# Performance work log

Hardware: AMD Instinct MI355X
Metric: run time of the kernel (lower is better)

Reference implementation:

```python
import jax, jax.numpy as jnp
import numpy as np

E = 1024
H = 16
D = E // H  # head dim


def setup_inputs() -> dict:
    key = jax.random.key(0)
    ks = jax.random.split(key, 8)
    N, L = 4, 2048
    x = jax.random.normal(ks[0], (N, L, E), dtype=jnp.float32)
    attn_mask = jnp.zeros((N, L), dtype=jnp.float32)  # additive mask
    s = 0.02
    Wq = jax.random.normal(ks[1], (E, E), dtype=jnp.float32) * s
    bq = jnp.zeros((E,), dtype=jnp.float32)
    Wk = jax.random.normal(ks[2], (E, E), dtype=jnp.float32) * s
    bk = jnp.zeros((E,), dtype=jnp.float32)
    Wv = jax.random.normal(ks[3], (E, E), dtype=jnp.float32) * s
    bv = jnp.zeros((E,), dtype=jnp.float32)
    return {"x": x, "attn_mask": attn_mask, "Wq": Wq, "bq": bq,
            "Wk": Wk, "bk": bk, "Wv": Wv, "bv": bv}


def _to_heads(t):
    N, L, _ = t.shape
    return t.reshape(N, L, H, D).transpose(0, 2, 1, 3)  # [N,H,L,D]


def reference(x, attn_mask, Wq, bq, Wk, bk, Wv, bv):
    # Linear projections (torch Linear: x @ W.T + b)
    Q = _to_heads(x @ Wq.T + bq) * (1.0 / jnp.sqrt(jnp.float32(D)))
    K = _to_heads(x @ Wk.T + bk)
    V = _to_heads(x @ Wv.T + bv)
    scores = jnp.einsum('nhqd,nhkd->nhqk', Q, K) + attn_mask[:, None, None, :]
    attn = jax.nn.softmax(scores, axis=-1)  # dropout p=0 -> identity
    out = jnp.einsum('nhqk,nhkd->nhqd', attn, V)  # [N,H,L,D]
    N, _, L, _ = out.shape
    return out.transpose(0, 2, 1, 3).reshape(N, L, E)
```

## Files before the change

kernel.cpp:

```cpp
#include <hip/hip_runtime.h>

#define DEV __device__ __forceinline__

typedef unsigned short u16;
typedef __attribute__((ext_vector_type(8))) __bf16 bf16x8;
typedef __attribute__((ext_vector_type(4))) float f32x4;
typedef __attribute__((ext_vector_type(16))) float f32x16;

#define LOG2E 1.44269504088896340736f

DEV u16 f2bf(float f) {
  union { float f; unsigned u; } v; v.f = f;
  unsigned r = v.u + 0x7FFFu + ((v.u >> 16) & 1u);
  return (u16)(r >> 16);
}

DEV float exp2_fast(float x) {
#if __has_builtin(__builtin_amdgcn_exp2f)
  return __builtin_amdgcn_exp2f(x);
#else
  return exp2f(x);
#endif
}

DEV float xor32_f(float v) { return __shfl_xor(v, 32, 64); }
DEV unsigned xor32_u(unsigned v) {
  return (unsigned)__shfl_xor((int)v, 32, 64);
}
DEV unsigned cvtpk_b(float lo, float hi) {
  union { float f; unsigned u; } a, b;
  a.f = lo; b.f = hi;
  return __builtin_amdgcn_perm(b.u + 0x8000u, a.u + 0x8000u, 0x07060302u);
}
DEV float bperm_f(int srclane, float v) {
  union { float f; int i; } u;
  u.f = v;
  u.i = __builtin_amdgcn_ds_bpermute(srclane * 4, u.i);
  return u.f;
}

template <typename T>
DEV void gload_lds16(const T* g, T* l) {
  __builtin_amdgcn_global_load_lds(
      (const __attribute__((address_space(1))) void*)(g),
      (__attribute__((address_space(3))) void*)(l),
      16, 0, 0);
}

DEV bf16x8 ldfrag(const u16* p) { return *(const bf16x8*)p; }

DEV void cast8(const float* __restrict__ in, u16* __restrict__ out) {
  float4 a = ((const float4*)in)[0];
  float4 b = ((const float4*)in)[1];
  uint4 o;
  o.x = (unsigned)f2bf(a.x) | ((unsigned)f2bf(a.y) << 16);
  o.y = (unsigned)f2bf(a.z) | ((unsigned)f2bf(a.w) << 16);
  o.z = (unsigned)f2bf(b.x) | ((unsigned)f2bf(b.y) << 16);
  o.w = (unsigned)f2bf(b.z) | ((unsigned)f2bf(b.w) << 16);
  *(uint4*)out = o;
}

__global__ __launch_bounds__(256) void prep_kernel(
    const float* __restrict__ x, const float* __restrict__ Wq,
    const float* __restrict__ Wk, const float* __restrict__ Wv,
    const float* __restrict__ mask,
    u16* __restrict__ xb, u16* __restrict__ wb, float* __restrict__ mlog) {
  const int i = blockIdx.x * 256 + threadIdx.x;
  const int NX = 8192 * 1024 / 8;
  const int NW = 1024 * 1024 / 8;
  if (i < NX) {
    cast8(x + (long)i * 8, xb + (long)i * 8);
  } else if (i < NX + 3 * NW) {
    int j = i - NX;
    int sel = j / NW;
    int jj = j - sel * NW;
    const float* W = (sel == 0) ? Wq : (sel == 1) ? Wk : Wv;
    cast8(W + (long)jj * 8, wb + (long)j * 8);
  } else {
    int j = i - NX - 3 * NW;
    float4 a = ((const float4*)mask)[2 * j];
    float4 b = ((const float4*)mask)[2 * j + 1];
    a.x *= LOG2E; a.y *= LOG2E; a.z *= LOG2E; a.w *= LOG2E;
    b.x *= LOG2E; b.y *= LOG2E; b.z *= LOG2E; b.w *= LOG2E;
    ((float4*)mlog)[2 * j] = a;
    ((float4*)mlog)[2 * j + 1] = b;
  }
}

__global__ __launch_bounds__(256) void qkv_gemm(
    const u16* __restrict__ xb, const u16* __restrict__ wb,
    const float* __restrict__ bq, const float* __restrict__ bk, const float* __restrict__ bv,
    u16* __restrict__ qb, u16* __restrict__ kb, u16* __restrict__ vtb) {
  __shared__ u16 As[128 * 64];
  __shared__ u16 Bs[128 * 64];
  const int t = threadIdx.x, lane = t & 63, w = t >> 6;
  const int wm = w >> 1, wn = w & 1;
  const int m0 = blockIdx.x * 128;
  const int cb = blockIdx.y;
  const int wsel = cb >> 3;
  const int n0 = (cb & 7) * 128;
  const u16* W = wb + wsel * (1024 * 1024);
  const float* bias = (wsel == 0) ? bq : (wsel == 1) ? bk : bv;
  const float scale = (wsel == 0) ? 0.125f * LOG2E : 1.0f;

  f32x4 acc[4][4];
  const f32x4 z4 = {0.f, 0.f, 0.f, 0.f};
  for (int i = 0; i < 4; ++i)
    for (int j = 0; j < 4; ++j) acc[i][j] = z4;

  const int srow = w * 32 + (lane >> 3);
  const int scol = (lane & 7) * 8;

  for (int k0 = 0; k0 < 1024; k0 += 64) {
    __syncthreads();
    for (int i = 0; i < 4; ++i) {
      gload_lds16(xb + (m0 + srow + i * 8) * 1024 + k0 + scol, &As[w * 2048 + i * 512]);
      gload_lds16(W + (n0 + srow + i * 8) * 1024 + k0 + scol, &Bs[w * 2048 + i * 512]);
    }
    __syncthreads();
    for (int ks = 0; ks < 2; ++ks) {
      bf16x8 a[4], b[4];
      for (int mi = 0; mi < 4; ++mi)
        a[mi] = ldfrag(&As[(wm * 64 + mi * 16 + (lane & 15)) * 64 + ks * 32 + (lane >> 4) * 8]);
      for (int ni = 0; ni < 4; ++ni)
        b[ni] = ldfrag(&Bs[(wn * 64 + ni * 16 + (lane & 15)) * 64 + ks * 32 + (lane >> 4) * 8]);
      for (int mi = 0; mi < 4; ++mi)
        for (int ni = 0; ni < 4; ++ni)
          acc[mi][ni] = __builtin_amdgcn_mfma_f32_16x16x32_bf16(a[mi], b[ni], acc[mi][ni], 0, 0, 0);
    }
  }
  if (wsel == 2) {
    for (int ni = 0; ni < 4; ++ni) {
      int col = n0 + wn * 64 + ni * 16 + (lane & 15);
      float bv_ = bias[col];
      int h = col >> 6, d = col & 63;
      for (int mi = 0; mi < 4; ++mi) {
        int gm = m0 + wm * 64 + mi * 16 + (lane >> 4) * 4;
        int nn = gm >> 11, lq = gm & 2047;
        ushort4 pk;
        pk.x = f2bf(acc[mi][ni][0] + bv_);
        pk.y = f2bf(acc[mi][ni][1] + bv_);
        pk.z = f2bf(acc[mi][ni][2] + bv_);
        pk.w = f2bf(acc[mi][ni][3] + bv_);
        *(ushort4*)(vtb + ((long)((nn << 4) + h) * 64 + d) * 2048 + lq) = pk;
      }
    }
  } else {
    u16* dst = (wsel == 0) ? qb : kb;
    for (int ni = 0; ni < 4; ++ni) {
      int col = n0 + wn * 64 + ni * 16 + (lane & 15);
      float bv_ = bias[col];
      int h = col >> 6, d = col & 63;
      for (int mi = 0; mi < 4; ++mi) {
        for (int r = 0; r < 4; ++r) {
          int gm = m0 + wm * 64 + mi * 16 + (lane >> 4) * 4 + r;
          int nn = gm >> 11, lq = gm & 2047;
          float val = acc[mi][ni][r] * scale + bv_;
          dst[(((nn << 4) + h) * 2048 + lq) * 64 + d] = f2bf(val);
        }
      }
    }
  }
}

__global__ __launch_bounds__(256) void flash_attn(
    const u16* __restrict__ qb, const u16* __restrict__ kb, const u16* __restrict__ vtb,
    const float* __restrict__ mlog, float* __restrict__ out) {
  __shared__ u16 SM[4][64 * 64];
  __shared__ float MK[2048];

  const int t = threadIdx.x, lane = t & 63, w = t >> 6;
  const int hi = lane >> 5, l31 = lane & 31;
  const int bid = blockIdx.x;
  const int swz = (bid & 7) * 128 + (bid >> 3);
  const int q0 = (swz & 15) * 128;
  const int head = swz >> 4;
  const int n = head >> 4, h = head & 15;

  const u16* qh = qb + head * (2048 * 64);
  const u16* kh = kb + head * (2048 * 64);
  const u16* vth = vtb + head * (64 * 2048);
  const float* mrow = mlog + n * 2048;

  const int srow8 = lane >> 3;
  const int scolsw = ((lane & 7) ^ srow8) * 8;
  const int rsw = (lane & 7) * 8;
  int fcolB[4];
  for (int dk = 0; dk < 4; ++dk) fcolB[dk] = (16 * dk + 8 * hi) ^ rsw;

  u16* QL = &SM[0][0];
  for (int i = 0; i < 4; ++i)
    gload_lds16(qh + (q0 + w * 32 + i * 8 + srow8) * 64 + scolsw, &QL[(w * 32 + i * 8) * 64]);
  for (int i = 0; i < 2; ++i) {
    int chunk = w * 2 + i;
    gload_lds16(mrow + chunk * 256 + lane * 4, &MK[chunk * 256]);
  }
  __syncthreads();
  bf16x8 qf[4];
  for (int dk = 0; dk < 4; ++dk)
    qf[dk] = ldfrag(&QL[(w * 32 + l31) * 64 + fcolB[dk]]);
  __syncthreads();

  {
    gload_lds16(kh + (w * 16 + srow8) * 64 + scolsw, &SM[0][w * 1024]);
    gload_lds16(kh + (w * 16 + 8 + srow8) * 64 + scolsw, &SM[0][w * 1024 + 512]);
    for (int i = 0; i < 2; ++i) {
      int dbase = w * 16 + i * 8;
      gload_lds16(vth + (dbase + srow8) * 2048 + scolsw, &SM[2][dbase * 64]);
    }
  }

  f32x16 o0, o1;
  for (int r = 0; r < 16; ++r) { o0[r] = 0.f; o1[r] = 0.f; }
  float lp = 0.f;

  for (int tt = 0; tt < 32; ++tt) {
    const int cur = tt & 1;
    const int kv0 = tt * 64;
    __syncthreads();

    if (tt < 31) {
      const int kv1 = kv0 + 64;
      const u16* ksrc = kh + kv1 * 64;
      gload_lds16(ksrc + (w * 16 + srow8) * 64 + scolsw, &SM[cur ^ 1][w * 1024]);
      gload_lds16(ksrc + (w * 16 + 8 + srow8) * 64 + scolsw, &SM[cur ^ 1][w * 1024 + 512]);
      for (int i = 0; i < 2; ++i) {
        int dbase = w * 16 + i * 8;
        gload_lds16(vth + (dbase + srow8) * 2048 + kv1 + scolsw, &SM[2 + (cur ^ 1)][dbase * 64]);
      }
    }
    const u16* Kc = &SM[cur][0];
    const u16* Vc = &SM[2 + cur][0];

    f32x16 s1, s2;
    {
      const float* mb = &MK[kv0 + 4 * hi];
      for (int mq = 0; mq < 4; ++mq) {
        f32x4 ma = *(const f32x4*)(mb + 8 * mq);
        f32x4 mc = *(const f32x4*)(mb + 32 + 8 * mq);
        for (int e = 0; e < 4; ++e) { s1[4 * mq + e] = ma[e]; s2[4 * mq + e] = mc[e]; }
      }
    }
    __builtin_amdgcn_s_setprio(1);
    for (int dk = 0; dk < 4; ++dk) {
      bf16x8 k0 = ldfrag(&Kc[l31 * 64 + fcolB[dk]]);
      bf16x8 k1 = ldfrag(&Kc[(32 + l31) * 64 + fcolB[dk]]);
      s1 = __builtin_amdgcn_mfma_f32_32x32x16_bf16(k0, qf[dk], s1, 0, 0, 0);
      s2 = __builtin_amdgcn_mfma_f32_32x32x16_bf16(k1, qf[dk], s2, 0, 0, 0);
    }
    __builtin_amdgcn_s_setprio(0);

#pragma unroll
    for (int r = 0; r < 16; ++r) {
      s1[r] = exp2_fast(s1[r]);
      s2[r] = exp2_fast(s2[r]);
    }

    float ts[16];
#pragma unroll
    for (int r = 0; r < 16; ++r) ts[r] = s1[r] + s2[r];
#pragma unroll
    for (int st = 8; st >= 1; st >>= 1)
#pragma unroll
      for (int r = 0; r < st; ++r) ts[r] += ts[r + st];
    lp += ts[0];

    unsigned raw[16];
#pragma unroll
    for (int mq = 0; mq < 8; ++mq) {
      raw[mq] = cvtpk_b(s1[2 * mq], s1[2 * mq + 1]);
      raw[8 + mq] = cvtpk_b(s2[2 * mq], s2[2 * mq + 1]);
    }
    union { unsigned u[16]; bf16x8 v[4]; } pw;
#pragma unroll
    for (int g = 0; g < 4; ++g) {
      unsigned a0 = raw[4 * g], a1 = raw[4 * g + 1];
      unsigned a2 = raw[4 * g + 2], a3 = raw[4 * g + 3];
      unsigned v0 = hi ? a0 : a2;
      unsigned v1 = hi ? a1 : a3;
      unsigned x0 = xor32_u(v0);
      unsigned x1 = xor32_u(v1);
      pw.u[4 * g + 0] = hi ? x0 : a0;
      pw.u[4 * g + 1] = hi ? x1 : a1;
      pw.u[4 * g + 2] = hi ? a2 : x0;
      pw.u[4 * g + 3] = hi ? a3 : x1;
    }

    __builtin_amdgcn_s_setprio(1);
    for (int kc = 0; kc < 4; ++kc) {
      bf16x8 bv0 = ldfrag(&Vc[l31 * 64 + fcolB[kc]]);
      bf16x8 bv1 = ldfrag(&Vc[(32 + l31) * 64 + fcolB[kc]]);
      o0 = __builtin_amdgcn_mfma_f32_32x32x16_bf16(pw.v[kc], bv0, o0, 0, 0, 0);
      o1 = __builtin_amdgcn_mfma_f32_32x32x16_bf16(pw.v[kc], bv1, o1, 0, 0, 0);
    }
    __builtin_amdgcn_s_setprio(0);
  }

  float lpf = lp + xor32_f(lp);
  float inv = 1.0f / lpf;
  for (int r = 0; r < 16; ++r) {
    int qrow = (r & 3) + 8 * (r >> 2) + 4 * hi;
    float invr = bperm_f(qrow, inv);
    int q = q0 + w * 32 + qrow;
    float* ob = out + (n * 2048 + q) * 1024 + h * 64;
    ob[l31] = o0[r] * invr;
    ob[32 + l31] = o1[r] * invr;
  }
}

extern "C" void kernel_launch(void* const* d_in, const int* in_sizes, int n_in,
                              void* d_out, int out_size, void* d_ws, size_t ws_size,
                              hipStream_t stream) {
  const float* x = (const float*)d_in[0];
  const float* mask = (const float*)d_in[1];
  const float* Wq = (const float*)d_in[2];
  const float* bq = (const float*)d_in[3];
  const float* Wk = (const float*)d_in[4];
  const float* bk = (const float*)d_in[5];
  const float* Wv = (const float*)d_in[6];
  const float* bv = (const float*)d_in[7];
  float* out = (float*)d_out;

  u16* xb = (u16*)d_ws;
  u16* wb = xb + 8192 * 1024;
  u16* qb = wb + 3 * 1024 * 1024;
  u16* kb = qb + 64 * 2048 * 64;
  u16* vtb = kb + 64 * 2048 * 64;
  float* mlog = (float*)(vtb + 64 * 2048 * 64);

  prep_kernel<<<1442816 / 256, 256, 0, stream>>>(x, Wq, Wk, Wv, mask, xb, wb, mlog);
  qkv_gemm<<<dim3(64, 24), 256, 0, stream>>>(xb, wb, bq, bk, bv, qb, kb, vtb);
  flash_attn<<<1024, 256, 0, stream>>>(qb, kb, vtb, mlog, out);
}
```

Baseline: 204.2 us.

## Double-buffer QKV GEMM loads and compute softmax row sums via MFMA

The QKV projection GEMM now uses a K-step of 32 with two LDS buffers. The next tile's global-to-LDS loads are issued before computing on the current tile, which removes one barrier per iteration and overlaps memory with MFMA work. In the attention kernel, the per-lane VALU reduction of exponentials plus the cross-lane shuffle and bpermute are replaced by an extra MFMA against a ones fragment. That MFMA accumulates row sums directly in the output layout. The trade is a third of additional matrix-core work in the PV stage, and the row sums now come from bf16-rounded probabilities.

```diff
diff --git a/kernel.cpp b/kernel.cpp
--- a/kernel.cpp
+++ b/kernel.cpp
@@ -23,7 +23,6 @@
 #endif
 }
 
-DEV float xor32_f(float v) { return __shfl_xor(v, 32, 64); }
 DEV unsigned xor32_u(unsigned v) {
   return (unsigned)__shfl_xor((int)v, 32, 64);
 }
@@ -31,12 +30,6 @@
   union { float f; unsigned u; } a, b;
   a.f = lo; b.f = hi;
   return __builtin_amdgcn_perm(b.u + 0x8000u, a.u + 0x8000u, 0x07060302u);
-}
-DEV float bperm_f(int srclane, float v) {
-  union { float f; int i; } u;
-  u.f = v;
-  u.i = __builtin_amdgcn_ds_bpermute(srclane * 4, u.i);
-  return u.f;
 }
 
 template <typename T>
@@ -48,6 +41,12 @@
 }
 
 DEV bf16x8 ldfrag(const u16* p) { return *(const bf16x8*)p; }
+
+DEV bf16x8 ones_frag() {
+  union { unsigned u[4]; bf16x8 v; } x;
+  x.u[0] = x.u[1] = x.u[2] = x.u[3] = 0x3F803F80u;
+  return x.v;
+}
 
 DEV void cast8(const float* __restrict__ in, u16* __restrict__ out) {
   float4 a = ((const float4*)in)[0];
@@ -91,8 +90,8 @@
     const u16* __restrict__ xb, const u16* __restrict__ wb,
     const float* __restrict__ bq, const float* __restrict__ bk, const float* __restrict__ bv,
     u16* __restrict__ qb, u16* __restrict__ kb, u16* __restrict__ vtb) {
-  __shared__ u16 As[128 * 64];
-  __shared__ u16 Bs[128 * 64];
+  __shared__ u16 As[2][128 * 32];
+  __shared__ u16 Bs[2][128 * 32];
   const int t = threadIdx.x, lane = t & 63, w = t >> 6;
   const int wm = w >> 1, wn = w & 1;
   const int m0 = blockIdx.x * 128;
@@ -108,26 +107,36 @@
   for (int i = 0; i < 4; ++i)
     for (int j = 0; j < 4; ++j) acc[i][j] = z4;
 
-  const int srow = w * 32 + (lane >> 3);
-  const int scol = (lane & 7) * 8;
-
-  for (int k0 = 0; k0 < 1024; k0 += 64) {
+  const int srow = w * 32 + (lane >> 2);
+  const int scol = (lane & 3) * 8;
+
+  for (int i = 0; i < 2; ++i) {
+    gload_lds16(xb + (m0 + srow + i * 16) * 1024 + scol, &As[0][(w * 32 + i * 16) * 32]);
+    gload_lds16(W + (n0 + srow + i * 16) * 1024 + scol, &Bs[0][(w * 32 + i * 16) * 32]);
+  }
+
+  for (int kt = 0; kt < 32; ++kt) {
+    const int cur = kt & 1;
     __syncthreads();
-    for (int i = 0; i < 4; ++i) {
-      gload_lds16(xb + (m0 + srow + i * 8) * 1024 + k0 + scol, &As[w * 2048 + i * 512]);
-      gload_lds16(W + (n0 + srow + i * 8) * 1024 + k0 + scol, &Bs[w * 2048 + i * 512]);
-    }
-    __syncthreads();
-    for (int ks = 0; ks < 2; ++ks) {
-      bf16x8 a[4], b[4];
-      for (int mi = 0; mi < 4; ++mi)
-        a[mi] = ldfrag(&As[(wm * 64 + mi * 16 + (lane & 15)) * 64 + ks * 32 + (lane >> 4) * 8]);
+    if (kt < 31) {
+      const int k1 = (kt + 1) * 32;
+      for (int i = 0; i < 2; ++i) {
+        gload_lds16(xb + (m0 + srow + i * 16) * 1024 + k1 + scol,
+                    &As[cur ^ 1][(w * 32 + i * 16) * 32]);
+        gload_lds16(W + (n0 + srow + i * 16) * 1024 + k1 + scol,
+                    &Bs[cur ^ 1][(w * 32 + i * 16) * 32]);
+      }
+    }
+    bf16x8 a[4], b[4];
+    for (int mi = 0; mi < 4; ++mi)
+      a[mi] = ldfrag(&As[cur][(wm * 64 + mi * 16 + (lane & 15)) * 32 + (lane >> 4) * 8]);
+    for (int ni = 0; ni < 4; ++ni)
+      b[ni] = ldfrag(&Bs[cur][(wn * 64 + ni * 16 + (lane & 15)) * 32 + (lane >> 4) * 8]);
+    __builtin_amdgcn_s_setprio(1);
+    for (int mi = 0; mi < 4; ++mi)
       for (int ni = 0; ni < 4; ++ni)
-        b[ni] = ldfrag(&Bs[(wn * 64 + ni * 16 + (lane & 15)) * 64 + ks * 32 + (lane >> 4) * 8]);
-      for (int mi = 0; mi < 4; ++mi)
-        for (int ni = 0; ni < 4; ++ni)
-          acc[mi][ni] = __builtin_amdgcn_mfma_f32_16x16x32_bf16(a[mi], b[ni], acc[mi][ni], 0, 0, 0);
-    }
+        acc[mi][ni] = __builtin_amdgcn_mfma_f32_16x16x32_bf16(a[mi], b[ni], acc[mi][ni], 0, 0, 0);
+    __builtin_amdgcn_s_setprio(0);
   }
   if (wsel == 2) {
     for (int ni = 0; ni < 4; ++ni) {
@@ -210,9 +219,9 @@
     }
   }
 
-  f32x16 o0, o1;
-  for (int r = 0; r < 16; ++r) { o0[r] = 0.f; o1[r] = 0.f; }
-  float lp = 0.f;
+  const bf16x8 ones = ones_frag();
+  f32x16 o0, o1, ls;
+  for (int r = 0; r < 16; ++r) { o0[r] = 0.f; o1[r] = 0.f; ls[r] = 0.f; }
 
   for (int tt = 0; tt < 32; ++tt) {
     const int cur = tt & 1;
@@ -255,15 +264,6 @@
       s1[r] = exp2_fast(s1[r]);
       s2[r] = exp2_fast(s2[r]);
     }
-
-    float ts[16];
-#pragma unroll
-    for (int r = 0; r < 16; ++r) ts[r] = s1[r] + s2[r];
-#pragma unroll
-    for (int st = 8; st >= 1; st >>= 1)
-#pragma unroll
-      for (int r = 0; r < st; ++r) ts[r] += ts[r + st];
-    lp += ts[0];
 
     unsigned raw[16];
 #pragma unroll
@@ -292,19 +292,18 @@
       bf16x8 bv1 = ldfrag(&Vc[(32 + l31) * 64 + fcolB[kc]]);
       o0 = __builtin_amdgcn_mfma_f32_32x32x16_bf16(pw.v[kc], bv0, o0, 0, 0, 0);
       o1 = __builtin_amdgcn_mfma_f32_32x32x16_bf16(pw.v[kc], bv1, o1, 0, 0, 0);
+      ls = __builtin_amdgcn_mfma_f32_32x32x16_bf16(pw.v[kc], ones, ls, 0, 0, 0);
     }
     __builtin_amdgcn_s_setprio(0);
   }
 
-  float lpf = lp + xor32_f(lp);
-  float inv = 1.0f / lpf;
   for (int r = 0; r < 16; ++r) {
+    float inv = 1.0f / ls[r];
     int qrow = (r & 3) + 8 * (r >> 2) + 4 * hi;
-    float invr = bperm_f(qrow, inv);
     int q = q0 + w * 32 + qrow;
     float* ob = out + (n * 2048 + q) * 1024 + h * 64;
-    ob[l31] = o0[r] * invr;
-    ob[32 + l31] = o1[r] * invr;
+    ob[l31] = o0[r] * inv;
+    ob[32 + l31] = o1[r] * inv;
   }
 }
 
```

Result: no change. 207.2 us (+1.5%).
